# Kernel optimization log

Hardware: AMD Instinct MI355X
Metric: run time of the kernel (lower is better)

Reference implementation:

```python
import jax, jax.numpy as jnp
import numpy as np

N = 50000
E_HALF = 800000
F_IN = 512
ATTN = 64
F_OUT = 256
TOL = 1e-5
MAXITER = 200


def setup_inputs() -> dict:
    key = jax.random.key(0)
    k1, k2, k3, k4, k5 = jax.random.split(key, 5)
    r0 = jax.random.randint(k1, (E_HALF,), 0, N)
    c0 = jax.random.randint(k2, (E_HALF,), 0, N)
    # symmetric edge list so the attention adjacency is self-adjoint (needed for CG)
    row = jnp.concatenate([r0, c0]).astype(jnp.int32)
    col = jnp.concatenate([c0, r0]).astype(jnp.int32)
    features = jax.random.normal(k3, (N, F_IN), dtype=jnp.float32)
    Wa = jax.random.normal(k4, (F_IN, ATTN), dtype=jnp.float32) / np.sqrt(F_IN)
    ba = jnp.zeros((ATTN,), dtype=jnp.float32)
    Wo = jax.random.normal(k5, (F_IN, F_OUT), dtype=jnp.float32) / np.sqrt(F_IN)
    bo = jnp.zeros((F_OUT,), dtype=jnp.float32)
    eps_inv = jnp.asarray(-2.0, dtype=jnp.float32)  # epsilon_sig_inv parameter
    return {"row": row, "col": col, "features": features,
            "Wa": Wa, "ba": ba, "Wo": Wo, "bo": bo, "eps_inv": eps_inv}


def reference(row, col, features, Wa, ba, Wo, bo, eps_inv):
    n = features.shape[0]
    # edge attention values
    attn = features @ Wa + ba                                   # [N, A]
    vals = jax.nn.sigmoid(jnp.einsum('ea,ea->e', attn[row], attn[col]))  # [E]
    # symmetric normalization: D^{-1/2} A D^{-1/2}
    deg = jax.ops.segment_sum(vals, row, num_segments=n)        # [N]
    dinv = jnp.where(deg > 0, jax.lax.rsqrt(jnp.where(deg > 0, deg, 1.0)), 0.0)
    nvals = vals * dinv[row] * dinv[col]                        # [E]
    epsilon = jax.nn.sigmoid(eps_inv)
    coef = 1.0 - epsilon
    # shifted Laplacian L = I - (1-eps) * Anorm ; matvec on [N, k]
    def Lmv(x):
        return x - coef * jax.ops.segment_sum(nvals[:, None] * x[col], row, num_segments=n)
    b = features @ Wo + bo                                      # [N, F_OUT]
    out, _ = jax.scipy.sparse.linalg.cg(Lmv, b, tol=TOL, maxiter=MAXITER)
    return out
```

## Files before the change

kernel.cpp:

```cpp
#include <hip/hip_runtime.h>
#include <math.h>

#define FIN 512
#define AD 64
#define FO 256
#define FO4 (FO / 4)
#define NCOMB 320
#define MAXIT_LAUNCH 12

#define S_GAM0 0
#define S_GAM1 1
#define S_PAP0 2
#define S_PAP1 3
#define S_BS   4
#define S_ATOL2 5
#define S_VV   6
#define S_BSP  7
#define S_SIG0 8
#define S_SIG1 9

typedef short bf16x8 __attribute__((ext_vector_type(8)));
typedef float f32x4 __attribute__((ext_vector_type(4)));

__device__ __forceinline__ double block_reduce256(double v) {
    __shared__ double sh[4];
    int lane = threadIdx.x & 63;
    int w = threadIdx.x >> 6;
#pragma unroll
    for (int s = 32; s; s >>= 1) v += __shfl_down(v, s, 64);
    if (lane == 0) sh[w] = v;
    __syncthreads();
    double r = 0.0;
    if (threadIdx.x == 0) r = sh[0] + sh[1] + sh[2] + sh[3];
    return r;
}

__device__ __forceinline__ unsigned short f2bf(float f) {
    unsigned int u = __float_as_uint(f);
    u = (u + 0x7FFFu + ((u >> 16) & 1u)) >> 16;
    return (unsigned short)u;
}
__device__ __forceinline__ float bf2f(unsigned short h) {
    return __uint_as_float(((unsigned int)h) << 16);
}

__global__ __launch_bounds__(256) void conv_bf_k(
    const float4* __restrict__ in, ushort4* __restrict__ out, int n4) {
    int i = blockIdx.x * 256 + threadIdx.x;
    if (i >= n4) return;
    float4 v = in[i];
    ushort4 h;
    h.x = f2bf(v.x); h.y = f2bf(v.y); h.z = f2bf(v.z); h.w = f2bf(v.w);
    out[i] = h;
}

__global__ __launch_bounds__(256) void packw_k(
    const float* __restrict__ Wa, const float* __restrict__ Wo,
    unsigned short* __restrict__ Bt) {
    int idx = blockIdx.x * 256 + threadIdx.x;
    if (idx >= NCOMB * FIN) return;
    int c = idx >> 9;
    int k = idx & 511;
    float v = (c < AD) ? Wa[(long)k * AD + c] : Wo[(long)k * FO + (c - AD)];
    Bt[idx] = f2bf(v);
}

__global__ __launch_bounds__(256) void gemm_mfma(
    const unsigned short* __restrict__ A,
    const unsigned short* __restrict__ Bt,
    const float* __restrict__ ba, const float* __restrict__ bo,
    float* __restrict__ attn, float* __restrict__ rvec, int M) {
    const int lane = threadIdx.x & 63;
    const int wid = threadIdx.x >> 6;
    const int l15 = lane & 15;
    const int lq = lane >> 4;
    const int rowBase = blockIdx.x * 64 + wid * 16;
    const int colBase = blockIdx.y * 64;
    int arow = rowBase + l15;
    if (arow >= M) arow = 0;
    const unsigned short* aptr = A + (size_t)arow * FIN + lq * 8;
    const unsigned short* bptr0 = Bt + (size_t)(colBase + l15) * FIN + lq * 8;
    f32x4 acc[4] = {};
#pragma unroll 4
    for (int k0 = 0; k0 < FIN; k0 += 32) {
        bf16x8 af = *(const bf16x8*)(aptr + k0);
#pragma unroll
        for (int c = 0; c < 4; ++c) {
            bf16x8 bf = *(const bf16x8*)(bptr0 + (size_t)c * 16 * FIN + k0);
            acc[c] = __builtin_amdgcn_mfma_f32_16x16x32_bf16(af, bf, acc[c], 0, 0, 0);
        }
    }
#pragma unroll
    for (int c = 0; c < 4; ++c) {
        int col = colBase + c * 16 + l15;
        float bv = (col < AD) ? ba[col] : bo[col - AD];
#pragma unroll
        for (int j = 0; j < 4; ++j) {
            int row = rowBase + lq * 4 + j;
            if (row < M) {
                float v = acc[c][j] + bv;
                if (col < AD) attn[(size_t)row * AD + col] = v;
                else rvec[(size_t)row * FO + (col - AD)] = v;
            }
        }
    }
}

__global__ __launch_bounds__(256) void edge_vals_k(
    const int* __restrict__ row, const int* __restrict__ col,
    const float* __restrict__ attn, float* __restrict__ vals,
    float* __restrict__ deg, int* __restrict__ cnt, int EH) {
    int g = blockIdx.x * blockDim.x + threadIdx.x;
    int e = g >> 3;
    int l = threadIdx.x & 7;
    if (e >= EH) return;
    int r = row[e], c = col[e];
    const float4* ar = (const float4*)&attn[(long)r * AD];
    const float4* ac = (const float4*)&attn[(long)c * AD];
    float4 x0 = ar[l * 2], x1 = ar[l * 2 + 1];
    float4 y0 = ac[l * 2], y1 = ac[l * 2 + 1];
    float a = x0.x * y0.x + x0.y * y0.y + x0.z * y0.z + x0.w * y0.w
            + x1.x * y1.x + x1.y * y1.y + x1.z * y1.z + x1.w * y1.w;
#pragma unroll
    for (int s = 4; s; s >>= 1) a += __shfl_down(a, s, 8);
    if (l == 0) {
        float v = 1.0f / (1.0f + __expf(-a));
        vals[e] = v;
        unsafeAtomicAdd(&deg[r], v);
        unsafeAtomicAdd(&deg[c], v);
        atomicAdd(&cnt[r], 1);
        atomicAdd(&cnt[c], 1);
    }
}

__global__ __launch_bounds__(256) void dinv_k(
    float* __restrict__ deg, float* __restrict__ sv, double* __restrict__ scal, int n) {
    int i = blockIdx.x * blockDim.x + threadIdx.x;
    double loc = 0.0;
    if (i < n) {
        float d = deg[i];
        sv[i] = d > 0.0f ? sqrtf(d) : 0.0f;
        deg[i] = d > 0.0f ? rsqrtf(d) : 0.0f;
        loc = (double)(d > 0.0f ? d : 0.0f);
    }
    double tot = block_reduce256(loc);
    if (threadIdx.x == 0) unsafeAtomicAdd(&scal[S_VV], tot);
}

__global__ __launch_bounds__(256) void vdotb_k(
    const float* __restrict__ b, const float* __restrict__ sv,
    double* __restrict__ vdotb, int n) {
    int j = threadIdx.x;
    int rpb = (n + gridDim.x - 1) / gridDim.x;
    int r0 = blockIdx.x * rpb;
    int r1 = r0 + rpb; if (r1 > n) r1 = n;
    double acc = 0.0;
    for (int i = r0; i < r1; ++i)
        acc += (double)sv[i] * (double)b[(size_t)i * FO + j];
    unsafeAtomicAdd(&vdotb[j], acc);
}

__global__ __launch_bounds__(256) void scan1_k(
    const int* __restrict__ cnt, int* __restrict__ rowptr, int* __restrict__ bsum, int n) {
    __shared__ int sh[256];
    int i = blockIdx.x * 256 + threadIdx.x;
    int v = (i < n) ? cnt[i] : 0;
    sh[threadIdx.x] = v;
    __syncthreads();
    for (int ofs = 1; ofs < 256; ofs <<= 1) {
        int t = (threadIdx.x >= ofs) ? sh[threadIdx.x - ofs] : 0;
        __syncthreads();
        sh[threadIdx.x] += t;
        __syncthreads();
    }
    if (i < n) rowptr[i] = sh[threadIdx.x] - v;
    if (threadIdx.x == 255) bsum[blockIdx.x] = sh[255];
}

__global__ __launch_bounds__(256) void scan2_k(int* bsum, int nb) {
    __shared__ int sh[256];
    int v = (threadIdx.x < nb) ? bsum[threadIdx.x] : 0;
    sh[threadIdx.x] = v;
    __syncthreads();
    for (int ofs = 1; ofs < 256; ofs <<= 1) {
        int t = (threadIdx.x >= ofs) ? sh[threadIdx.x - ofs] : 0;
        __syncthreads();
        sh[threadIdx.x] += t;
        __syncthreads();
    }
    if (threadIdx.x < nb) bsum[threadIdx.x] = sh[threadIdx.x] - v;
}

__global__ __launch_bounds__(256) void scan3_k(
    int* __restrict__ rowptr, const int* __restrict__ bsum, int n, int E) {
    int i = blockIdx.x * 256 + threadIdx.x;
    if (i < n) rowptr[i] += bsum[blockIdx.x];
    if (i == 0) rowptr[n] = E;
}

__global__ void scatter_k(
    const int* __restrict__ row, const int* __restrict__ col,
    const float* __restrict__ vals, const float* __restrict__ dinv,
    const int* __restrict__ rowptr, int* __restrict__ cursor,
    int2* __restrict__ csr_cw, int EH) {
    int e = blockIdx.x * blockDim.x + threadIdx.x;
    if (e >= EH) return;
    int r = row[e], c = col[e];
    int wbits = __float_as_int(vals[e] * dinv[r] * dinv[c]);
    int pos1 = rowptr[r] + atomicAdd(&cursor[r], 1);
    csr_cw[pos1] = make_int2(c, wbits);
    int pos2 = rowptr[c] + atomicAdd(&cursor[c], 1);
    csr_cw[pos2] = make_int2(r, wbits);
}

__global__ __launch_bounds__(256) void cg_init(
    float4* __restrict__ r4, ushort4* __restrict__ pb4,
    float4* __restrict__ x4, const float* __restrict__ sv,
    const double* __restrict__ vdotb, double* __restrict__ scal,
    const float* __restrict__ eps_inv, int total4) {
    const float epsv = 1.0f / (1.0f + __expf(-eps_inv[0]));
    const double vv = scal[S_VV];
    const double inv_vv = (vv > 0.0) ? 1.0 / vv : 0.0;
    double lorig = 0.0, lperp = 0.0;
    int stride = gridDim.x * blockDim.x;
    for (int i = blockIdx.x * blockDim.x + threadIdx.x; i < total4; i += stride) {
        int rowi = i >> 6;
        int c0 = (i & 63) << 2;
        float vi = sv[rowi];
        float4 b = r4[i];
        lorig += (double)(b.x * b.x + b.y * b.y + b.z * b.z + b.w * b.w);
        float s0 = (float)(vdotb[c0 + 0] * inv_vv);
        float s1 = (float)(vdotb[c0 + 1] * inv_vv);
        float s2 = (float)(vdotb[c0 + 2] * inv_vv);
        float s3 = (float)(vdotb[c0 + 3] * inv_vv);
        float4 bp = make_float4(b.x - s0 * vi, b.y - s1 * vi,
                                b.z - s2 * vi, b.w - s3 * vi);
        r4[i] = bp;
        ushort4 h;
        h.x = f2bf(bp.x); h.y = f2bf(bp.y); h.z = f2bf(bp.z); h.w = f2bf(bp.w);
        pb4[i] = h;
        float vie = vi / epsv;
        x4[i] = make_float4(s0 * vie, s1 * vie, s2 * vie, s3 * vie);
        lperp += (double)(bp.x * bp.x + bp.y * bp.y + bp.z * bp.z + bp.w * bp.w);
    }
    double t1 = block_reduce256(lorig);
    if (threadIdx.x == 0) unsafeAtomicAdd(&scal[S_BS], t1);
    __syncthreads();
    double t2 = block_reduce256(lperp);
    if (threadIdx.x == 0) unsafeAtomicAdd(&scal[S_BSP], t2);
}

__global__ void cg_init2(double* scal) {
    if (threadIdx.x == 0 && blockIdx.x == 0) {
        scal[S_GAM0] = scal[S_BSP];
        scal[S_ATOL2] = 1e-10 * scal[S_BS];
    }
}

__global__ __launch_bounds__(256) void cg_spmm(
    const int* __restrict__ rowptr, const int2* __restrict__ csr_cw,
    const ushort4* __restrict__ pb4, float4* __restrict__ ap4,
    double* __restrict__ scal, const int* __restrict__ flag,
    const float* __restrict__ eps_inv, int n, int it) {
    if (*flag) return;
    const float coef = 1.0f / (1.0f + __expf(eps_inv[0]));
    const int lane = threadIdx.x & 63;
    const int rowi = (blockIdx.x << 2) + (threadIdx.x >> 6);
    double dacc = 0.0, sacc = 0.0;
    if (rowi < n) {
        int js = rowptr[rowi], je = rowptr[rowi + 1];
        float4 acc = make_float4(0.f, 0.f, 0.f, 0.f);
        for (int j0 = js; j0 < je; j0 += 64) {
            int rem = je - j0;
            int cj = 0;
            float wj = 0.0f;
            if (lane < rem) {
                int2 cw = csr_cw[j0 + lane];
                cj = cw.x;
                wj = __int_as_float(cw.y);
            }
            int cntc = rem < 64 ? rem : 64;
            int cnt8 = (cntc + 7) & ~7;
            for (int t = 0; t < cnt8; t += 8) {
                float ww[8];
                ushort4 vv[8];
#pragma unroll
                for (int u = 0; u < 8; ++u) {
                    int c = __shfl(cj, t + u, 64);
                    ww[u] = __shfl(wj, t + u, 64);
                    vv[u] = pb4[c * FO4 + lane];
                }
#pragma unroll
                for (int u = 0; u < 8; ++u) {
                    acc.x += ww[u] * bf2f(vv[u].x);
                    acc.y += ww[u] * bf2f(vv[u].y);
                    acc.z += ww[u] * bf2f(vv[u].z);
                    acc.w += ww[u] * bf2f(vv[u].w);
                }
            }
        }
        ushort4 ph = pb4[rowi * FO4 + lane];
        float4 pv = make_float4(bf2f(ph.x), bf2f(ph.y), bf2f(ph.z), bf2f(ph.w));
        float4 ap;
        ap.x = pv.x - coef * acc.x;
        ap.y = pv.y - coef * acc.y;
        ap.z = pv.z - coef * acc.z;
        ap.w = pv.w - coef * acc.w;
        ap4[rowi * FO4 + lane] = ap;
        dacc = (double)(pv.x * ap.x + pv.y * ap.y + pv.z * ap.z + pv.w * ap.w);
        sacc = (double)(ap.x * ap.x + ap.y * ap.y + ap.z * ap.z + ap.w * ap.w);
    }
    double t1 = block_reduce256(dacc);
    if (threadIdx.x == 0) unsafeAtomicAdd(&scal[S_PAP0 + (it & 1)], t1);
    __syncthreads();
    double t2 = block_reduce256(sacc);
    if (threadIdx.x == 0) unsafeAtomicAdd(&scal[S_SIG0 + (it & 1)], t2);
}

__global__ __launch_bounds__(256) void cg_fused(
    float4* __restrict__ x4, float4* __restrict__ r4, ushort4* __restrict__ pb4,
    const float4* __restrict__ ap4, double* __restrict__ scal, int* __restrict__ flag,
    int total4, int it) {
    if (*flag) return;
    const double gamma = scal[it & 1];
    const double pap = scal[S_PAP0 + (it & 1)];
    const double sig = scal[S_SIG0 + (it & 1)];
    const double alpha_d = gamma / pap;
    const double gnew = alpha_d * alpha_d * sig - gamma;
    const float alpha = (float)alpha_d;
    const float beta = (float)(gnew / gamma);
    if (blockIdx.x == 0 && threadIdx.x == 0) {
        scal[(it + 1) & 1] = gnew;
        scal[S_PAP0 + ((it + 1) & 1)] = 0.0;
        scal[S_SIG0 + ((it + 1) & 1)] = 0.0;
        if (gnew <= scal[S_ATOL2]) *flag = 1;
    }
    int stride = gridDim.x * blockDim.x;
    for (int i = blockIdx.x * blockDim.x + threadIdx.x; i < total4; i += stride) {
        float4 av = ap4[i], rv = r4[i], xv = x4[i];
        ushort4 ph = pb4[i];
        float4 pv = make_float4(bf2f(ph.x), bf2f(ph.y), bf2f(ph.z), bf2f(ph.w));
        xv.x += alpha * pv.x; xv.y += alpha * pv.y;
        xv.z += alpha * pv.z; xv.w += alpha * pv.w;
        rv.x -= alpha * av.x; rv.y -= alpha * av.y;
        rv.z -= alpha * av.z; rv.w -= alpha * av.w;
        x4[i] = xv; r4[i] = rv;
        pv.x = rv.x + beta * pv.x; pv.y = rv.y + beta * pv.y;
        pv.z = rv.z + beta * pv.z; pv.w = rv.w + beta * pv.w;
        ushort4 h;
        h.x = f2bf(pv.x); h.y = f2bf(pv.y); h.z = f2bf(pv.z); h.w = f2bf(pv.w);
        pb4[i] = h;
    }
}

extern "C" void kernel_launch(void* const* d_in, const int* in_sizes, int n_in,
                              void* d_out, int out_size, void* d_ws, size_t ws_size,
                              hipStream_t stream) {
    const int* row = (const int*)d_in[0];
    const int* col = (const int*)d_in[1];
    const float* feat = (const float*)d_in[2];
    const float* Wa = (const float*)d_in[3];
    const float* ba = (const float*)d_in[4];
    const float* Wo = (const float*)d_in[5];
    const float* bo = (const float*)d_in[6];
    const float* eps_inv = (const float*)d_in[7];
    const int E = in_sizes[0];
    const int EH = E / 2;
    const int n = in_sizes[2] / FIN;
    const int total4 = n * FO4;
    const int nscanb = (n + 255) / 256;

    char* w = (char*)d_ws;
    size_t off = 0;
    auto alloc = [&](size_t bytes) -> void* {
        void* p = w + off;
        off += (bytes + 255) & ~(size_t)255;
        return p;
    };
    float* r_vec = (float*)alloc((size_t)n * FO * 4);
    float* ap_vec = (float*)alloc((size_t)n * FO * 4);
    ushort4* p_bf = (ushort4*)alloc((size_t)n * FO * 2);
    float* attn = (float*)alloc((size_t)n * AD * 4);
    float* vals = (float*)alloc((size_t)EH * 4);
    int2* csr_cw = (int2*)alloc((size_t)E * 8);
    int* rowptr = (int*)alloc((size_t)(n + 1) * 4);
    int* bsum = (int*)alloc((size_t)nscanb * 4);
    unsigned short* Bt = (unsigned short*)alloc((size_t)NCOMB * FIN * 2);
    float* sv = (float*)alloc((size_t)n * 4);
    size_t zb_bytes = (size_t)n * 12 + 128 + 16 + 2048;
    char* zb = (char*)alloc(zb_bytes);
    float* deg = (float*)zb;
    int* cnt = (int*)(zb + (size_t)n * 4);
    int* cursor = (int*)(zb + (size_t)n * 8);
    double* scal = (double*)(zb + (size_t)n * 12);
    int* flag = (int*)(zb + (size_t)n * 12 + 128);
    double* vdotb = (double*)(zb + (size_t)n * 12 + 128 + 16);

    unsigned short* feat_bf = (unsigned short*)ap_vec;

    hipMemsetAsync(zb, 0, zb_bytes, stream);

    int nconv4 = n * (FIN / 4);
    conv_bf_k<<<(nconv4 + 255) / 256, 256, 0, stream>>>((const float4*)feat,
                                                        (ushort4*)feat_bf, nconv4);
    packw_k<<<(NCOMB * FIN + 255) / 256, 256, 0, stream>>>(Wa, Wo, Bt);
    dim3 gg((n + 63) / 64, NCOMB / 64);
    gemm_mfma<<<gg, 256, 0, stream>>>(feat_bf, Bt, ba, bo, attn, r_vec, n);

    edge_vals_k<<<((size_t)EH * 8 + 255) / 256, 256, 0, stream>>>(row, col, attn, vals,
                                                                  deg, cnt, EH);
    dinv_k<<<(n + 255) / 256, 256, 0, stream>>>(deg, sv, scal, n);
    vdotb_k<<<256, 256, 0, stream>>>(r_vec, sv, vdotb, n);
    scan1_k<<<nscanb, 256, 0, stream>>>(cnt, rowptr, bsum, n);
    scan2_k<<<1, 256, 0, stream>>>(bsum, nscanb);
    scan3_k<<<nscanb, 256, 0, stream>>>(rowptr, bsum, n, E);
    scatter_k<<<(EH + 255) / 256, 256, 0, stream>>>(row, col, vals, deg, rowptr, cursor,
                                                    csr_cw, EH);

    float4* x4 = (float4*)d_out;
    cg_init<<<2048, 256, 0, stream>>>((float4*)r_vec, p_bf, x4,
                                      sv, vdotb, scal, eps_inv, total4);
    cg_init2<<<1, 64, 0, stream>>>(scal);

    int spmm_blocks = (n + 3) / 4;
    for (int it = 0; it < MAXIT_LAUNCH; ++it) {
        cg_spmm<<<spmm_blocks, 256, 0, stream>>>(rowptr, csr_cw, (const ushort4*)p_bf,
                                                 (float4*)ap_vec, scal, flag, eps_inv, n, it);
        cg_fused<<<2048, 256, 0, stream>>>(x4, (float4*)r_vec, p_bf,
                                           (const float4*)ap_vec, scal, flag, total4, it);
    }
}
```

Measured before the change: 1.689 ms.

## Bucket CSR neighbors by column chunk to improve gather locality in SpMM

Each row's neighbor list is now grouped into 16 buckets by column index (col >> 12). Counts, scan and scatter work on a per-row-per-bucket array, and a two-level scan replaces the single-level one. Neighbors within a row come out roughly sorted by column, so concurrent SpMM rows gather the bf16 p vectors from similar regions and should get better cache locality. The cost is a 16x larger count/cursor array, a larger memset and extra scan launches in setup.

Measured after the change: 1.753 ms. 3.8% more time.

```diff
diff --git a/kernel.cpp b/kernel.cpp
--- a/kernel.cpp
+++ b/kernel.cpp
@@ -7,6 +7,8 @@
 #define FO4 (FO / 4)
 #define NCOMB 320
 #define MAXIT_LAUNCH 12
+#define CSH 12
+#define NCH 16
 
 #define S_GAM0 0
 #define S_GAM1 1
@@ -109,7 +111,7 @@
 __global__ __launch_bounds__(256) void edge_vals_k(
     const int* __restrict__ row, const int* __restrict__ col,
     const float* __restrict__ attn, float* __restrict__ vals,
-    float* __restrict__ deg, int* __restrict__ cnt, int EH) {
+    float* __restrict__ deg, int* __restrict__ cnt2, int EH) {
     int g = blockIdx.x * blockDim.x + threadIdx.x;
     int e = g >> 3;
     int l = threadIdx.x & 7;
@@ -128,8 +130,8 @@
         vals[e] = v;
         unsafeAtomicAdd(&deg[r], v);
         unsafeAtomicAdd(&deg[c], v);
-        atomicAdd(&cnt[r], 1);
-        atomicAdd(&cnt[c], 1);
+        atomicAdd(&cnt2[r * NCH + (c >> CSH)], 1);
+        atomicAdd(&cnt2[c * NCH + (r >> CSH)], 1);
     }
 }
 
@@ -161,10 +163,10 @@
 }
 
 __global__ __launch_bounds__(256) void scan1_k(
-    const int* __restrict__ cnt, int* __restrict__ rowptr, int* __restrict__ bsum, int n) {
+    const int* __restrict__ in, int* __restrict__ out, int* __restrict__ bsum, int len) {
     __shared__ int sh[256];
     int i = blockIdx.x * 256 + threadIdx.x;
-    int v = (i < n) ? cnt[i] : 0;
+    int v = (i < len) ? in[i] : 0;
     sh[threadIdx.x] = v;
     __syncthreads();
     for (int ofs = 1; ofs < 256; ofs <<= 1) {
@@ -173,7 +175,7 @@
         sh[threadIdx.x] += t;
         __syncthreads();
     }
-    if (i < n) rowptr[i] = sh[threadIdx.x] - v;
+    if (i < len) out[i] = sh[threadIdx.x] - v;
     if (threadIdx.x == 255) bsum[blockIdx.x] = sh[255];
 }
 
@@ -192,24 +194,26 @@
 }
 
 __global__ __launch_bounds__(256) void scan3_k(
-    int* __restrict__ rowptr, const int* __restrict__ bsum, int n, int E) {
+    int* __restrict__ arr, const int* __restrict__ bsum, int len, int total) {
     int i = blockIdx.x * 256 + threadIdx.x;
-    if (i < n) rowptr[i] += bsum[blockIdx.x];
-    if (i == 0) rowptr[n] = E;
+    if (i < len) arr[i] += bsum[blockIdx.x];
+    if (i == 0 && total >= 0) arr[len] = total;
 }
 
 __global__ void scatter_k(
     const int* __restrict__ row, const int* __restrict__ col,
     const float* __restrict__ vals, const float* __restrict__ dinv,
-    const int* __restrict__ rowptr, int* __restrict__ cursor,
+    const int* __restrict__ rp2, int* __restrict__ cursor2,
     int2* __restrict__ csr_cw, int EH) {
     int e = blockIdx.x * blockDim.x + threadIdx.x;
     if (e >= EH) return;
     int r = row[e], c = col[e];
     int wbits = __float_as_int(vals[e] * dinv[r] * dinv[c]);
-    int pos1 = rowptr[r] + atomicAdd(&cursor[r], 1);
+    int s1 = r * NCH + (c >> CSH);
+    int pos1 = rp2[s1] + atomicAdd(&cursor2[s1], 1);
     csr_cw[pos1] = make_int2(c, wbits);
-    int pos2 = rowptr[c] + atomicAdd(&cursor[c], 1);
+    int s2 = c * NCH + (r >> CSH);
+    int pos2 = rp2[s2] + atomicAdd(&cursor2[s2], 1);
     csr_cw[pos2] = make_int2(r, wbits);
 }
 
@@ -258,7 +262,7 @@
 }
 
 __global__ __launch_bounds__(256) void cg_spmm(
-    const int* __restrict__ rowptr, const int2* __restrict__ csr_cw,
+    const int* __restrict__ rp2, const int2* __restrict__ csr_cw,
     const ushort4* __restrict__ pb4, float4* __restrict__ ap4,
     double* __restrict__ scal, const int* __restrict__ flag,
     const float* __restrict__ eps_inv, int n, int it) {
@@ -268,7 +272,7 @@
     const int rowi = (blockIdx.x << 2) + (threadIdx.x >> 6);
     double dacc = 0.0, sacc = 0.0;
     if (rowi < n) {
-        int js = rowptr[rowi], je = rowptr[rowi + 1];
+        int js = rp2[rowi * NCH], je = rp2[rowi * NCH + NCH];
         float4 acc = make_float4(0.f, 0.f, 0.f, 0.f);
         for (int j0 = js; j0 < je; j0 += 64) {
             int rem = je - j0;
@@ -368,7 +372,9 @@
     const int EH = E / 2;
     const int n = in_sizes[2] / FIN;
     const int total4 = n * FO4;
-    const int nscanb = (n + 255) / 256;
+    const int len2 = n * NCH;
+    const int ns1 = (len2 + 255) / 256;
+    const int ns2 = (ns1 + 255) / 256;
 
     char* w = (char*)d_ws;
     size_t off = 0;
@@ -383,18 +389,19 @@
     float* attn = (float*)alloc((size_t)n * AD * 4);
     float* vals = (float*)alloc((size_t)EH * 4);
     int2* csr_cw = (int2*)alloc((size_t)E * 8);
-    int* rowptr = (int*)alloc((size_t)(n + 1) * 4);
-    int* bsum = (int*)alloc((size_t)nscanb * 4);
+    int* rp2 = (int*)alloc((size_t)(len2 + 1) * 4);
+    int* bsA = (int*)alloc((size_t)ns1 * 4);
+    int* bsB = (int*)alloc((size_t)ns2 * 4);
     unsigned short* Bt = (unsigned short*)alloc((size_t)NCOMB * FIN * 2);
     float* sv = (float*)alloc((size_t)n * 4);
-    size_t zb_bytes = (size_t)n * 12 + 128 + 16 + 2048;
+    size_t zb_bytes = (size_t)n * 4 + (size_t)len2 * 8 + 128 + 16 + 2048;
     char* zb = (char*)alloc(zb_bytes);
     float* deg = (float*)zb;
-    int* cnt = (int*)(zb + (size_t)n * 4);
-    int* cursor = (int*)(zb + (size_t)n * 8);
-    double* scal = (double*)(zb + (size_t)n * 12);
-    int* flag = (int*)(zb + (size_t)n * 12 + 128);
-    double* vdotb = (double*)(zb + (size_t)n * 12 + 128 + 16);
+    int* cnt2 = (int*)(zb + (size_t)n * 4);
+    int* cursor2 = (int*)(zb + (size_t)n * 4 + (size_t)len2 * 4);
+    double* scal = (double*)(zb + (size_t)n * 4 + (size_t)len2 * 8);
+    int* flag = (int*)(zb + (size_t)n * 4 + (size_t)len2 * 8 + 128);
+    double* vdotb = (double*)(zb + (size_t)n * 4 + (size_t)len2 * 8 + 128 + 16);
 
     unsigned short* feat_bf = (unsigned short*)ap_vec;
 
@@ -408,13 +415,15 @@
     gemm_mfma<<<gg, 256, 0, stream>>>(feat_bf, Bt, ba, bo, attn, r_vec, n);
 
     edge_vals_k<<<((size_t)EH * 8 + 255) / 256, 256, 0, stream>>>(row, col, attn, vals,
-                                                                  deg, cnt, EH);
+                                                                  deg, cnt2, EH);
     dinv_k<<<(n + 255) / 256, 256, 0, stream>>>(deg, sv, scal, n);
     vdotb_k<<<256, 256, 0, stream>>>(r_vec, sv, vdotb, n);
-    scan1_k<<<nscanb, 256, 0, stream>>>(cnt, rowptr, bsum, n);
-    scan2_k<<<1, 256, 0, stream>>>(bsum, nscanb);
-    scan3_k<<<nscanb, 256, 0, stream>>>(rowptr, bsum, n, E);
-    scatter_k<<<(EH + 255) / 256, 256, 0, stream>>>(row, col, vals, deg, rowptr, cursor,
+    scan1_k<<<ns1, 256, 0, stream>>>(cnt2, rp2, bsA, len2);
+    scan1_k<<<ns2, 256, 0, stream>>>(bsA, bsA, bsB, ns1);
+    scan2_k<<<1, 256, 0, stream>>>(bsB, ns2);
+    scan3_k<<<ns2, 256, 0, stream>>>(bsA, bsB, ns1, -1);
+    scan3_k<<<ns1, 256, 0, stream>>>(rp2, bsA, len2, E);
+    scatter_k<<<(EH + 255) / 256, 256, 0, stream>>>(row, col, vals, deg, rp2, cursor2,
                                                     csr_cw, EH);
 
     float4* x4 = (float4*)d_out;
@@ -424,7 +433,7 @@
 
     int spmm_blocks = (n + 3) / 4;
     for (int it = 0; it < MAXIT_LAUNCH; ++it) {
-        cg_spmm<<<spmm_blocks, 256, 0, stream>>>(rowptr, csr_cw, (const ushort4*)p_bf,
+        cg_spmm<<<spmm_blocks, 256, 0, stream>>>(rp2, csr_cw, (const ushort4*)p_bf,
                                                  (float4*)ap_vec, scal, flag, eps_inv, n, it);
         cg_fused<<<2048, 256, 0, stream>>>(x4, (float4*)r_vec, p_bf,
                                            (const float4*)ap_vec, scal, flag, total4, it);
```
